# Kernel tuning notes

Hardware: AMD Instinct MI355X
Metric: run time of the kernel (lower is better)

Reference implementation:

```python
import jax, jax.numpy as jnp
import numpy as np
import math

B, S, D = 4, 1024, 1024
E, DE = 8, 128            # n_experts, expert_dim (D == E*DE)
TOPK = 2
SCALE = 1.0 / math.sqrt(D)  # source divides by sqrt(self.dim) = sqrt(transformer_dim)


def setup_inputs() -> dict:
    key = jax.random.key(0)
    k1, k2, k3, k4, k5 = jax.random.split(key, 5)
    Q = jax.random.normal(k1, (B, S, D), dtype=jnp.float32)
    K = jax.random.normal(k2, (B, S, D), dtype=jnp.float32)
    V = jax.random.normal(k3, (B, S, D), dtype=jnp.float32)
    route_prob = jax.random.uniform(k4, (B, E), dtype=jnp.float32)
    # first-stage MoE dispatch (idx_list): expert_mask[e, b] == 1 iff batch b routed to expert e
    expert_mask = jax.random.randint(k5, (E, B), 0, 2).astype(jnp.int32)
    mask = jnp.ones((B, S), dtype=jnp.float32)  # accepted but unused by the source forward
    return {"Q": Q, "K": K, "V": V, "route_prob": route_prob,
            "expert_mask": expert_mask, "mask": mask}


def reference(Q, K, V, route_prob, expert_mask, mask):
    # RowParallelMatmulWithMoE: each expert e attends using its 128-wide feature slice
    Qe = Q.reshape(B, S, E, DE)
    Ke = K.reshape(B, S, E, DE)
    scores = jnp.einsum('bsed,bted->ebst', Qe, Ke) * SCALE   # [E, B, S, S]
    probs = jax.nn.softmax(scores, axis=-1)                   # per-expert softmax (dropout p=0)
    # index_add_ scatter: sum routed experts' attention maps per batch element
    m1 = expert_mask.astype(Q.dtype)                          # [E, B]
    attn = jnp.einsum('eb,ebst->bst', m1, probs)              # [B, S, S]
    # preprocess: top-k expert re-selection from route_prob -> new idx_list
    _, top_idx = jax.lax.top_k(route_prob, TOPK)              # [B, TOPK]
    m2 = jnp.zeros((B, E), dtype=Q.dtype).at[jnp.arange(B)[:, None], top_idx].set(1.0)
    # ColumnParallelMatmulWithMoE: attn @ V restricted to each selected expert's V slice
    Ve = V.reshape(B, S, E, DE)
    out = jnp.einsum('bst,bted->bsed', attn, Ve) * m2[:, None, :, None]  # [B, S, E, DE]
    return out.reshape(B, S, D)
```

## Files before the change

kernel.cpp:

```cpp
#include <hip/hip_runtime.h>
#include <hip/hip_bf16.h>
#include <stdint.h>

#define B_ 4
#define S_ 1024
#define E_ 8
#define DE_ 128
#define SCALE_ 0.03125f

typedef __attribute__((ext_vector_type(8))) short short8;
typedef __attribute__((ext_vector_type(4))) float f32x4;
typedef unsigned short ushort_t;
typedef unsigned int uint32;
typedef unsigned long long u64;
typedef unsigned char uchar;

__device__ __forceinline__ ushort_t f2bf(float f) {
    uint32 u = __float_as_uint(f);
    uint32 r = u + 0x7fffu + ((u >> 16) & 1u);
    return (ushort_t)(r >> 16);
}

__device__ __forceinline__ uchar f2fp8(float f) {
    float a = fminf(fmaxf(f, -448.f), 448.f);
    uint32 u = __float_as_uint(a);
    uint32 s = (u >> 31) << 7;
    int ex = (int)((u >> 23) & 0xff);
    uint32 man = u & 0x7fffff;
    int e8 = ex - 127 + 7;
    if (e8 >= 1) {
        uint32 m = man >> 20;
        uint32 rem = man & 0xfffff;
        if (rem > 0x80000u || (rem == 0x80000u && (m & 1))) ++m;
        if (m == 8) { m = 0; ++e8; }
        if (e8 > 15) { e8 = 15; m = 6; }
        return (uchar)(s | ((uint32)e8 << 3) | m);
    } else {
        int m = (int)rintf(fabsf(a) * 512.f);
        if (m > 7) m = 7;
        return (uchar)(s | (uint32)m);
    }
}

#define GLOAD_LDS16(g, l) __builtin_amdgcn_global_load_lds( \
    (const __attribute__((address_space(1))) unsigned int*)(g), \
    (__attribute__((address_space(3))) unsigned int*)(l), 16, 0, 0)

__device__ __forceinline__ void stageK32(const uchar* g, uchar* lds, int tid) {
    #pragma unroll
    for (int k2 = 0; k2 < 4; ++k2) {
        int u = tid + k2 * 512;
        int r = u >> 3, c = u & 7;
        int cc = c ^ (r & 7);
        GLOAD_LDS16(g + r * 128 + (cc << 4), lds + (u << 4));
    }
}
__device__ __forceinline__ void stageV32(const uchar* g, uchar* lds, int tid) {
    #pragma unroll
    for (int k2 = 0; k2 < 4; ++k2) {
        int u = tid + k2 * 512;
        int r = u >> 4, c = u & 15;
        int cc = (c & 8) | ((c & 7) ^ (r & 7));
        GLOAD_LDS16(g + (size_t)r * 2048 + (cc << 4), lds + (u << 4));
    }
}
__device__ __forceinline__ void stageQ(const uchar* g, uchar* lds, int tid) {
    if (tid < 128) {
        int r = tid >> 3, c = tid & 7;
        int cc = c ^ (r & 7);
        GLOAD_LDS16(g + r * 128 + (cc << 4), lds + (tid << 4));
    }
}
__device__ __forceinline__ u64 fld8(const uchar* lds, int row, int kk, int quad) {
    int c = kk * 2 + (quad >> 1);
    int phys = c ^ (row & 7);
    return *(const u64*)(lds + row * 128 + (phys << 4) + ((quad & 1) << 3));
}
__device__ __forceinline__ short8 fldv(const uchar* lds, int row, int kk, int quad) {
    int c = kk * 4 + quad;
    int phys = (c & 8) | ((c & 7) ^ (row & 7));
    return *(const short8*)(lds + (size_t)row * 256 + (phys << 4));
}

__device__ __forceinline__ void top2(const float* rp, int& i1, int& i2) {
    float v1 = rp[0]; i1 = 0;
    #pragma unroll
    for (int i = 1; i < 8; ++i) { float v = rp[i]; if (v > v1) { v1 = v; i1 = i; } }
    float v2 = -1e30f; i2 = 0;
    #pragma unroll
    for (int i = 0; i < 8; ++i) {
        if (i == i1) continue;
        float v = rp[i]; if (v > v2) { v2 = v; i2 = i; }
    }
}

__global__ __launch_bounds__(256) void prep_kernel(
        const float* __restrict__ Q, const float* __restrict__ K,
        const float* __restrict__ V, const float* __restrict__ route,
        const int* __restrict__ em,
        uchar* __restrict__ Qb, uchar* __restrict__ Kb,
        ushort_t* __restrict__ Vt, float* __restrict__ out) {
    __shared__ ushort_t tile[64][130];
    const int tid = threadIdx.x;
    const int sc = blockIdx.x, e = blockIdx.y, b = blockIdx.z;
    const int s0 = sc * 64;
    const size_t plane8 = ((size_t)(b * 8 + e)) << 17;

    const bool ak = em[e * B_ + b] != 0;
    int i1, i2; top2(route + b * 8, i1, i2);
    const bool av = (e == i1) || (e == i2);

    if (!av) {
        #pragma unroll
        for (int i = 0; i < 8; ++i) {
            int idx = tid + i * 256, r = idx >> 5, c4 = idx & 31;
            *(float4*)(out + (((size_t)(b * 1024 + s0 + r)) << 10) + (e << 7) + (c4 << 2))
                = make_float4(0.f, 0.f, 0.f, 0.f);
        }
    }
    if (ak) {
        #pragma unroll
        for (int i = 0; i < 2; ++i) {
            int u = tid + i * 256;
            int r = u >> 3, dg = u & 7;
            const float* qs = Q + ((size_t)(b * 1024 + s0 + r) << 10) + (e << 7) + (dg << 4);
            const float* ks = K + ((size_t)(b * 1024 + s0 + r) << 10) + (e << 7) + (dg << 4);
            union { uint4 w; uchar c[16]; } oq, ok;
            #pragma unroll
            for (int j = 0; j < 4; ++j) {
                float4 qv = ((const float4*)qs)[j];
                float4 kv = ((const float4*)ks)[j];
                oq.c[j*4+0] = f2fp8(qv.x); oq.c[j*4+1] = f2fp8(qv.y);
                oq.c[j*4+2] = f2fp8(qv.z); oq.c[j*4+3] = f2fp8(qv.w);
                ok.c[j*4+0] = f2fp8(kv.x); ok.c[j*4+1] = f2fp8(kv.y);
                ok.c[j*4+2] = f2fp8(kv.z); ok.c[j*4+3] = f2fp8(kv.w);
            }
            size_t oo = plane8 + ((size_t)(s0 + r) << 7) + (dg << 4);
            *(uint4*)(Qb + oo) = oq.w;
            *(uint4*)(Kb + oo) = ok.w;
        }
    }
    if (av) {
        #pragma unroll
        for (int i = 0; i < 8; ++i) {
            int idx = tid + i * 256, r = idx >> 5, c4 = idx & 31;
            size_t in_off = ((size_t)(b * 1024 + s0 + r) << 10) + (e << 7) + (c4 << 2);
            float4 v = *(const float4*)(V + in_off);
            ushort_t* p = &tile[r][c4 << 2];
            p[0] = f2bf(v.x); p[1] = f2bf(v.y); p[2] = f2bf(v.z); p[3] = f2bf(v.w);
        }
        __syncthreads();
        #pragma unroll
        for (int i = 0; i < 4; ++i) {
            int item = tid + i * 256, d = item & 127, sg = item >> 7;
            union { uint4 q; ushort_t u[8]; } tmp;
            #pragma unroll
            for (int j = 0; j < 8; ++j) tmp.u[j] = tile[sg * 8 + j][d];
            *(uint4*)(Vt + (((size_t)(b * 8 + e)) << 17) + (((size_t)d) << 10)
                      + s0 + (sg << 3)) = tmp.q;
        }
    }
}

__global__ __launch_bounds__(512, 1) void attn_mega(
        const uchar* __restrict__ Qb, const uchar* __restrict__ Kb,
        const ushort_t* __restrict__ Vt, const float* __restrict__ route,
        const int* __restrict__ em, float* __restrict__ out) {

    __shared__ __align__(16) uchar kt[2][32768];
    __shared__ __align__(16) uchar qt[2][2048];
    __shared__ __align__(16) uchar attnL[32768];
    __shared__ float red[8][16];

    const int stile = blockIdx.x, b = blockIdx.y;
    const int s0 = stile * 16;
    const int tid = threadIdx.x;
    const int w = tid >> 6, lane = tid & 63;
    const int quad = lane >> 4, l16 = lane & 15;

    uint32 epack = 0; int ne = 0;
    #pragma unroll
    for (int e = 0; e < 8; ++e)
        if (em[e * B_ + b] != 0) { epack |= (uint32)e << (3 * ne); ++ne; }
    int i1, i2; top2(route + b * 8, i1, i2);

    f32x4 aacc[4][2];
    #pragma unroll
    for (int c = 0; c < 4; ++c)
        #pragma unroll
        for (int n = 0; n < 2; ++n) aacc[c][n] = (f32x4){0.f, 0.f, 0.f, 0.f};

    if (ne > 0) {
        int e0 = epack & 7;
        stageQ(Qb + (((size_t)(b * 8 + e0)) << 17) + ((size_t)s0 << 7), qt[0], tid);
        stageK32(Kb + (((size_t)(b * 8 + e0)) << 17), kt[0], tid);
        __syncthreads();

        for (int i = 0; i < ne; ++i) {
            int e = (epack >> (3 * i)) & 7;
            const uchar* kp = Kb + (((size_t)(b * 8 + e)) << 17);

            u64 af[4];
            #pragma unroll
            for (int kk = 0; kk < 4; ++kk) af[kk] = fld8(qt[i & 1], l16, kk, quad);

            float rsum[4] = {0.f, 0.f, 0.f, 0.f};
            f32x4 ps[4][2];

            #pragma unroll
            for (int c = 0; c < 4; ++c) {
                int g = i * 4 + c;
                if (c < 3) {
                    stageK32(kp + (size_t)(c + 1) * 32768, kt[(g + 1) & 1], tid);
                } else if (i + 1 < ne) {
                    int en = (epack >> (3 * (i + 1))) & 7;
                    stageQ(Qb + (((size_t)(b * 8 + en)) << 17) + ((size_t)s0 << 7),
                           qt[(i + 1) & 1], tid);
                    stageK32(Kb + (((size_t)(b * 8 + en)) << 17), kt[(g + 1) & 1], tid);
                } else {
                    stageV32((const uchar*)(Vt + (((size_t)(b * 8 + i1)) << 17)),
                             kt[(g + 1) & 1], tid);
                }
                const uchar* kb = kt[g & 1];
                #pragma unroll
                for (int n = 0; n < 2; ++n) {
                    f32x4 s = {0.f, 0.f, 0.f, 0.f};
                    int trow = w * 32 + n * 16 + l16;
                    #pragma unroll
                    for (int kk = 0; kk < 4; ++kk) {
                        u64 bf = fld8(kb, trow, kk, quad);
                        s = __builtin_amdgcn_mfma_f32_16x16x32_fp8_fp8(
                            (long)af[kk], (long)bf, s, 0, 0, 0);
                    }
                    #pragma unroll
                    for (int r = 0; r < 4; ++r) {
                        float p = __expf(s[r] * SCALE_);
                        ps[c][n][r] = p;
                        rsum[r] += p;
                    }
                }
                __syncthreads();
            }

            #pragma unroll
            for (int off = 1; off < 16; off <<= 1)
                #pragma unroll
                for (int r = 0; r < 4; ++r) rsum[r] += __shfl_xor(rsum[r], off, 64);
            if (l16 == 0) {
                #pragma unroll
                for (int r = 0; r < 4; ++r) red[w][quad * 4 + r] = rsum[r];
            }
            __syncthreads();
            float rinv[4];
            #pragma unroll
            for (int r = 0; r < 4; ++r) {
                float l = 0.f;
                #pragma unroll
                for (int ww = 0; ww < 8; ++ww) l += red[ww][quad * 4 + r];
                rinv[r] = 1.0f / l;
            }
            #pragma unroll
            for (int c = 0; c < 4; ++c)
                #pragma unroll
                for (int n = 0; n < 2; ++n)
                    #pragma unroll
                    for (int r = 0; r < 4; ++r)
                        aacc[c][n][r] += ps[c][n][r] * rinv[r];
        }
    } else {
        stageV32((const uchar*)(Vt + (((size_t)(b * 8 + i1)) << 17)), kt[0], tid);
    }

    #pragma unroll
    for (int c = 0; c < 4; ++c)
        #pragma unroll
        for (int n = 0; n < 2; ++n)
            #pragma unroll
            for (int r = 0; r < 4; ++r) {
                int row = quad * 4 + r;
                int t = c * 256 + w * 32 + n * 16 + l16;
                int ct = t >> 3;
                int phys = (ct & ~7) | ((ct & 7) ^ (row & 7));
                *(ushort_t*)(attnL + row * 2048 + (phys << 4) + ((t & 7) << 1)) =
                    f2bf(aacc[c][n][r]);
            }
    __syncthreads();

    int selE[2] = {i1, i2};
    #pragma unroll
    for (int sel = 0; sel < 2; ++sel) {
        const uchar* vp = (const uchar*)(Vt + (((size_t)(b * 8 + selE[sel])) << 17));
        f32x4 oacc = {0.f, 0.f, 0.f, 0.f};
        #pragma unroll
        for (int c = 0; c < 8; ++c) {
            int g = ne * 4 + sel * 8 + c;
            if (c < 7)
                stageV32(vp + (size_t)(c + 1) * 256, kt[(g + 1) & 1], tid);
            else if (sel == 0)
                stageV32((const uchar*)(Vt + (((size_t)(b * 8 + selE[1])) << 17)),
                         kt[(g + 1) & 1], tid);
            const uchar* vb = kt[g & 1];
            #pragma unroll
            for (int kk = 0; kk < 4; ++kk) {
                int ct = c * 16 + kk * 4 + quad;
                int phys = (ct & ~7) | ((ct & 7) ^ (l16 & 7));
                short8 afr = *(const short8*)(attnL + l16 * 2048 + (phys << 4));
                short8 bfr = fldv(vb, w * 16 + l16, kk, quad);
                oacc = __builtin_amdgcn_mfma_f32_16x16x32_bf16(afr, bfr, oacc, 0, 0, 0);
            }
            __syncthreads();
        }
        #pragma unroll
        for (int r = 0; r < 4; ++r)
            out[(((size_t)(b * 1024 + s0 + quad * 4 + r)) << 10)
                + selE[sel] * 128 + w * 16 + l16] = oacc[r];
    }
}

extern "C" void kernel_launch(void* const* d_in, const int* in_sizes, int n_in,
                              void* d_out, int out_size, void* d_ws, size_t ws_size,
                              hipStream_t stream) {
    const float* Q     = (const float*)d_in[0];
    const float* K     = (const float*)d_in[1];
    const float* V     = (const float*)d_in[2];
    const float* route = (const float*)d_in[3];
    const int*   em    = (const int*)d_in[4];
    float* out = (float*)d_out;

    const size_t NB = (size_t)B_ * E_ * S_ * DE_;
    uchar* Qb = (uchar*)d_ws;
    uchar* Kb = Qb + NB;
    ushort_t* Vt = (ushort_t*)(Kb + NB);

    dim3 gp(16, 8, 4);
    prep_kernel<<<gp, 256, 0, stream>>>(Q, K, V, route, em, Qb, Kb, Vt, out);
    dim3 gm(64, 4);
    attn_mega<<<gm, 512, 0, stream>>>(Qb, Kb, Vt, route, em, out);
}
```

Measured before the change: 135.8 us.

## Triple-buffer K/V staging with vmcnt-based waits and preload all Q tiles

Moves from a double-buffered LDS ring to a triple-buffered one that keeps two stages in flight. Each stage waits with s_waitcnt vmcnt(4) plus a raw s_barrier instead of a full __syncthreads, so the next global-to-LDS load no longer waits for all loads to drain. All routed experts' Q tiles are loaded up front with 4-byte LDS-direct loads spread over all threads, and output stores are deferred to the end. This uses more LDS (96KB ring plus 16KB Q), and correctness depends on the hand-counted vmcnt matching the per-thread load count.

```diff
diff --git a/kernel.cpp b/kernel.cpp
--- a/kernel.cpp
+++ b/kernel.cpp
@@ -45,6 +45,9 @@
 #define GLOAD_LDS16(g, l) __builtin_amdgcn_global_load_lds( \
     (const __attribute__((address_space(1))) unsigned int*)(g), \
     (__attribute__((address_space(3))) unsigned int*)(l), 16, 0, 0)
+#define GLOAD_LDS4(g, l) __builtin_amdgcn_global_load_lds( \
+    (const __attribute__((address_space(1))) unsigned int*)(g), \
+    (__attribute__((address_space(3))) unsigned int*)(l), 4, 0, 0)
 
 __device__ __forceinline__ void stageK32(const uchar* g, uchar* lds, int tid) {
     #pragma unroll
@@ -64,12 +67,12 @@
         GLOAD_LDS16(g + (size_t)r * 2048 + (cc << 4), lds + (u << 4));
     }
 }
-__device__ __forceinline__ void stageQ(const uchar* g, uchar* lds, int tid) {
-    if (tid < 128) {
-        int r = tid >> 3, c = tid & 7;
-        int cc = c ^ (r & 7);
-        GLOAD_LDS16(g + r * 128 + (cc << 4), lds + (tid << 4));
-    }
+__device__ __forceinline__ void stageQ4(const uchar* g, uchar* lds, int tid) {
+    int r = tid >> 5;
+    int ct = (tid >> 2) & 7;
+    int bo = (tid & 3) << 2;
+    int cc = ct ^ (r & 7);
+    GLOAD_LDS4(g + r * 128 + (cc << 4) + bo, lds + (tid << 2));
 }
 __device__ __forceinline__ u64 fld8(const uchar* lds, int row, int kk, int quad) {
     int c = kk * 2 + (quad >> 1);
@@ -167,8 +170,8 @@
         const ushort_t* __restrict__ Vt, const float* __restrict__ route,
         const int* __restrict__ em, float* __restrict__ out) {
 
-    __shared__ __align__(16) uchar kt[2][32768];
-    __shared__ __align__(16) uchar qt[2][2048];
+    __shared__ __align__(16) uchar kt3[3 * 32768];
+    __shared__ __align__(16) uchar qAll[16384];
     __shared__ __align__(16) uchar attnL[32768];
     __shared__ float red[8][16];
 
@@ -184,91 +187,109 @@
         if (em[e * B_ + b] != 0) { epack |= (uint32)e << (3 * ne); ++ne; }
     int i1, i2; top2(route + b * 8, i1, i2);
 
+    const int tk = ne * 4;
+    const int G = tk + 16;
+
     f32x4 aacc[4][2];
     #pragma unroll
     for (int c = 0; c < 4; ++c)
         #pragma unroll
         for (int n = 0; n < 2; ++n) aacc[c][n] = (f32x4){0.f, 0.f, 0.f, 0.f};
 
-    if (ne > 0) {
-        int e0 = epack & 7;
-        stageQ(Qb + (((size_t)(b * 8 + e0)) << 17) + ((size_t)s0 << 7), qt[0], tid);
-        stageK32(Kb + (((size_t)(b * 8 + e0)) << 17), kt[0], tid);
-        __syncthreads();
-
-        for (int i = 0; i < ne; ++i) {
-            int e = (epack >> (3 * i)) & 7;
-            const uchar* kp = Kb + (((size_t)(b * 8 + e)) << 17);
-
-            u64 af[4];
-            #pragma unroll
-            for (int kk = 0; kk < 4; ++kk) af[kk] = fld8(qt[i & 1], l16, kk, quad);
-
-            float rsum[4] = {0.f, 0.f, 0.f, 0.f};
-            f32x4 ps[4][2];
-
-            #pragma unroll
-            for (int c = 0; c < 4; ++c) {
-                int g = i * 4 + c;
-                if (c < 3) {
-                    stageK32(kp + (size_t)(c + 1) * 32768, kt[(g + 1) & 1], tid);
-                } else if (i + 1 < ne) {
-                    int en = (epack >> (3 * (i + 1))) & 7;
-                    stageQ(Qb + (((size_t)(b * 8 + en)) << 17) + ((size_t)s0 << 7),
-                           qt[(i + 1) & 1], tid);
-                    stageK32(Kb + (((size_t)(b * 8 + en)) << 17), kt[(g + 1) & 1], tid);
-                } else {
-                    stageV32((const uchar*)(Vt + (((size_t)(b * 8 + i1)) << 17)),
-                             kt[(g + 1) & 1], tid);
+    int ib = 0;
+    int cb = 0;
+
+    auto issue = [&](int g) {
+        uchar* buf = kt3 + (size_t)ib * 32768u;
+        if (g < tk) {
+            int e = (epack >> (3 * (g >> 2))) & 7;
+            stageK32(Kb + (((size_t)(b * 8 + e)) << 17) + (size_t)(g & 3) * 32768,
+                     buf, tid);
+        } else {
+            int v = g - tk;
+            int e = (v >> 3) ? i2 : i1;
+            stageV32((const uchar*)(Vt + (((size_t)(b * 8 + e)) << 17))
+                         + (size_t)(v & 7) * 256,
+                     buf, tid);
+        }
+        ib = (ib == 2) ? 0 : ib + 1;
+    };
+    auto pipe = [&](int g) {
+        if (g + 1 < G) asm volatile("s_waitcnt vmcnt(4)" ::: "memory");
+        else           asm volatile("s_waitcnt vmcnt(0)" ::: "memory");
+        __builtin_amdgcn_s_barrier();
+        __builtin_amdgcn_sched_barrier(0);
+        if (g + 2 < G) issue(g + 2);
+    };
+
+    for (int i = 0; i < ne; ++i) {
+        int e = (epack >> (3 * i)) & 7;
+        stageQ4(Qb + (((size_t)(b * 8 + e)) << 17) + ((size_t)s0 << 7),
+                qAll + i * 2048, tid);
+    }
+    issue(0); issue(1);
+
+    for (int i = 0; i < ne; ++i) {
+        const uchar* qp = qAll + i * 2048;
+        u64 af[4];
+        float rsum[4] = {0.f, 0.f, 0.f, 0.f};
+        f32x4 ps[4][2];
+
+        #pragma unroll
+        for (int c = 0; c < 4; ++c) {
+            int g = i * 4 + c;
+            pipe(g);
+            if (c == 0) {
+                #pragma unroll
+                for (int kk = 0; kk < 4; ++kk) af[kk] = fld8(qp, l16, kk, quad);
+            }
+            const uchar* kb = kt3 + (size_t)cb * 32768u;
+            cb = (cb == 2) ? 0 : cb + 1;
+            #pragma unroll
+            for (int n = 0; n < 2; ++n) {
+                f32x4 s = {0.f, 0.f, 0.f, 0.f};
+                int trow = w * 32 + n * 16 + l16;
+                #pragma unroll
+                for (int kk = 0; kk < 4; ++kk) {
+                    u64 bf = fld8(kb, trow, kk, quad);
+                    s = __builtin_amdgcn_mfma_f32_16x16x32_fp8_fp8(
+                        (long)af[kk], (long)bf, s, 0, 0, 0);
                 }
-                const uchar* kb = kt[g & 1];
                 #pragma unroll
-                for (int n = 0; n < 2; ++n) {
-                    f32x4 s = {0.f, 0.f, 0.f, 0.f};
-                    int trow = w * 32 + n * 16 + l16;
-                    #pragma unroll
-                    for (int kk = 0; kk < 4; ++kk) {
-                        u64 bf = fld8(kb, trow, kk, quad);
-                        s = __builtin_amdgcn_mfma_f32_16x16x32_fp8_fp8(
-                            (long)af[kk], (long)bf, s, 0, 0, 0);
-                    }
-                    #pragma unroll
-                    for (int r = 0; r < 4; ++r) {
-                        float p = __expf(s[r] * SCALE_);
-                        ps[c][n][r] = p;
-                        rsum[r] += p;
-                    }
+                for (int r = 0; r < 4; ++r) {
+                    float p = __expf(s[r] * SCALE_);
+                    ps[c][n][r] = p;
+                    rsum[r] += p;
                 }
-                __syncthreads();
-            }
-
-            #pragma unroll
-            for (int off = 1; off < 16; off <<= 1)
+            }
+        }
+
+        #pragma unroll
+        for (int off = 1; off < 16; off <<= 1)
+            #pragma unroll
+            for (int r = 0; r < 4; ++r) rsum[r] += __shfl_xor(rsum[r], off, 64);
+        if (l16 == 0) {
+            #pragma unroll
+            for (int r = 0; r < 4; ++r) red[w][quad * 4 + r] = rsum[r];
+        }
+        asm volatile("s_waitcnt lgkmcnt(0)" ::: "memory");
+        __builtin_amdgcn_s_barrier();
+        __builtin_amdgcn_sched_barrier(0);
+        float rinv[4];
+        #pragma unroll
+        for (int r = 0; r < 4; ++r) {
+            float l = 0.f;
+            #pragma unroll
+            for (int ww = 0; ww < 8; ++ww) l += red[ww][quad * 4 + r];
+            rinv[r] = 1.0f / l;
+        }
+        #pragma unroll
+        for (int c = 0; c < 4; ++c)
+            #pragma unroll
+            for (int n = 0; n < 2; ++n)
                 #pragma unroll
-                for (int r = 0; r < 4; ++r) rsum[r] += __shfl_xor(rsum[r], off, 64);
-            if (l16 == 0) {
-                #pragma unroll
-                for (int r = 0; r < 4; ++r) red[w][quad * 4 + r] = rsum[r];
-            }
-            __syncthreads();
-            float rinv[4];
-            #pragma unroll
-            for (int r = 0; r < 4; ++r) {
-                float l = 0.f;
-                #pragma unroll
-                for (int ww = 0; ww < 8; ++ww) l += red[ww][quad * 4 + r];
-                rinv[r] = 1.0f / l;
-            }
-            #pragma unroll
-            for (int c = 0; c < 4; ++c)
-                #pragma unroll
-                for (int n = 0; n < 2; ++n)
-                    #pragma unroll
-                    for (int r = 0; r < 4; ++r)
-                        aacc[c][n][r] += ps[c][n][r] * rinv[r];
-        }
-    } else {
-        stageV32((const uchar*)(Vt + (((size_t)(b * 8 + i1)) << 17)), kt[0], tid);
+                for (int r = 0; r < 4; ++r)
+                    aacc[c][n][r] += ps[c][n][r] * rinv[r];
     }
 
     #pragma unroll
@@ -284,37 +305,40 @@
                 *(ushort_t*)(attnL + row * 2048 + (phys << 4) + ((t & 7) << 1)) =
                     f2bf(aacc[c][n][r]);
             }
-    __syncthreads();
+    asm volatile("s_waitcnt lgkmcnt(0)" ::: "memory");
+    __builtin_amdgcn_s_barrier();
+    __builtin_amdgcn_sched_barrier(0);
 
     int selE[2] = {i1, i2};
+    f32x4 oacc[2];
+    #pragma unroll
+    for (int sel = 0; sel < 2; ++sel) oacc[sel] = (f32x4){0.f, 0.f, 0.f, 0.f};
+
     #pragma unroll
     for (int sel = 0; sel < 2; ++sel) {
-        const uchar* vp = (const uchar*)(Vt + (((size_t)(b * 8 + selE[sel])) << 17));
-        f32x4 oacc = {0.f, 0.f, 0.f, 0.f};
         #pragma unroll
         for (int c = 0; c < 8; ++c) {
-            int g = ne * 4 + sel * 8 + c;
-            if (c < 7)
-                stageV32(vp + (size_t)(c + 1) * 256, kt[(g + 1) & 1], tid);
-            else if (sel == 0)
-                stageV32((const uchar*)(Vt + (((size_t)(b * 8 + selE[1])) << 17)),
-                         kt[(g + 1) & 1], tid);
-            const uchar* vb = kt[g & 1];
+            int g = tk + sel * 8 + c;
+            pipe(g);
+            const uchar* vb = kt3 + (size_t)cb * 32768u;
+            cb = (cb == 2) ? 0 : cb + 1;
             #pragma unroll
             for (int kk = 0; kk < 4; ++kk) {
                 int ct = c * 16 + kk * 4 + quad;
                 int phys = (ct & ~7) | ((ct & 7) ^ (l16 & 7));
                 short8 afr = *(const short8*)(attnL + l16 * 2048 + (phys << 4));
                 short8 bfr = fldv(vb, w * 16 + l16, kk, quad);
-                oacc = __builtin_amdgcn_mfma_f32_16x16x32_bf16(afr, bfr, oacc, 0, 0, 0);
-            }
-            __syncthreads();
-        }
+                oacc[sel] = __builtin_amdgcn_mfma_f32_16x16x32_bf16(
+                    afr, bfr, oacc[sel], 0, 0, 0);
+            }
+        }
+    }
+    #pragma unroll
+    for (int sel = 0; sel < 2; ++sel)
         #pragma unroll
         for (int r = 0; r < 4; ++r)
             out[(((size_t)(b * 1024 + s0 + quad * 4 + r)) << 10)
-                + selE[sel] * 128 + w * 16 + l16] = oacc[r];
-    }
+                + selE[sel] * 128 + w * 16 + l16] = oacc[sel][r];
 }
 
 extern "C" void kernel_launch(void* const* d_in, const int* in_sizes, int n_in,
```

Result: no change. 135.3 us (-0.3%).

## Load K, Q and V MFMA fragments directly from global memory, dropping LDS staging

Applied to the files above, without the earlier changes.

Removes the double-buffered LDS staging of K, Q and V tiles (global_load_lds plus swizzled LDS reads and per-chunk barriers) and has each lane load its MFMA fragments straight from global memory. This cuts LDS usage from about 100KB to about 33KB and removes most __syncthreads. The softmax reduction buffer is double-buffered so no trailing barrier is needed. The cost is that global loads are now 8 or 16 bytes per lane with strided rows, they are no longer prefetched ahead of compute, and any reuse across waves has to come from the L1/L2 caches.

```diff
diff --git a/kernel.cpp b/kernel.cpp
--- a/kernel.cpp
+++ b/kernel.cpp
@@ -42,46 +42,6 @@
     }
 }
 
-#define GLOAD_LDS16(g, l) __builtin_amdgcn_global_load_lds( \
-    (const __attribute__((address_space(1))) unsigned int*)(g), \
-    (__attribute__((address_space(3))) unsigned int*)(l), 16, 0, 0)
-
-__device__ __forceinline__ void stageK32(const uchar* g, uchar* lds, int tid) {
-    #pragma unroll
-    for (int k2 = 0; k2 < 4; ++k2) {
-        int u = tid + k2 * 512;
-        int r = u >> 3, c = u & 7;
-        int cc = c ^ (r & 7);
-        GLOAD_LDS16(g + r * 128 + (cc << 4), lds + (u << 4));
-    }
-}
-__device__ __forceinline__ void stageV32(const uchar* g, uchar* lds, int tid) {
-    #pragma unroll
-    for (int k2 = 0; k2 < 4; ++k2) {
-        int u = tid + k2 * 512;
-        int r = u >> 4, c = u & 15;
-        int cc = (c & 8) | ((c & 7) ^ (r & 7));
-        GLOAD_LDS16(g + (size_t)r * 2048 + (cc << 4), lds + (u << 4));
-    }
-}
-__device__ __forceinline__ void stageQ(const uchar* g, uchar* lds, int tid) {
-    if (tid < 128) {
-        int r = tid >> 3, c = tid & 7;
-        int cc = c ^ (r & 7);
-        GLOAD_LDS16(g + r * 128 + (cc << 4), lds + (tid << 4));
-    }
-}
-__device__ __forceinline__ u64 fld8(const uchar* lds, int row, int kk, int quad) {
-    int c = kk * 2 + (quad >> 1);
-    int phys = c ^ (row & 7);
-    return *(const u64*)(lds + row * 128 + (phys << 4) + ((quad & 1) << 3));
-}
-__device__ __forceinline__ short8 fldv(const uchar* lds, int row, int kk, int quad) {
-    int c = kk * 4 + quad;
-    int phys = (c & 8) | ((c & 7) ^ (row & 7));
-    return *(const short8*)(lds + (size_t)row * 256 + (phys << 4));
-}
-
 __device__ __forceinline__ void top2(const float* rp, int& i1, int& i2) {
     float v1 = rp[0]; i1 = 0;
     #pragma unroll
@@ -167,10 +127,8 @@
         const ushort_t* __restrict__ Vt, const float* __restrict__ route,
         const int* __restrict__ em, float* __restrict__ out) {
 
-    __shared__ __align__(16) uchar kt[2][32768];
-    __shared__ __align__(16) uchar qt[2][2048];
     __shared__ __align__(16) uchar attnL[32768];
-    __shared__ float red[8][16];
+    __shared__ float red[2][8][16];
 
     const int stile = blockIdx.x, b = blockIdx.y;
     const int s0 = stile * 16;
@@ -190,85 +148,67 @@
         #pragma unroll
         for (int n = 0; n < 2; ++n) aacc[c][n] = (f32x4){0.f, 0.f, 0.f, 0.f};
 
-    if (ne > 0) {
-        int e0 = epack & 7;
-        stageQ(Qb + (((size_t)(b * 8 + e0)) << 17) + ((size_t)s0 << 7), qt[0], tid);
-        stageK32(Kb + (((size_t)(b * 8 + e0)) << 17), kt[0], tid);
+    for (int i = 0; i < ne; ++i) {
+        int e = (epack >> (3 * i)) & 7;
+        const uchar* kp = Kb + (((size_t)(b * 8 + e)) << 17);
+        const uchar* qp = Qb + (((size_t)(b * 8 + e)) << 17) + ((size_t)s0 << 7)
+                          + l16 * 128 + quad * 8;
+
+        u64 af[4];
+        #pragma unroll
+        for (int kk = 0; kk < 4; ++kk) af[kk] = *(const u64*)(qp + kk * 32);
+
+        float rsum[4] = {0.f, 0.f, 0.f, 0.f};
+        f32x4 ps[4][2];
+
+        #pragma unroll
+        for (int c = 0; c < 4; ++c) {
+            #pragma unroll
+            for (int n = 0; n < 2; ++n) {
+                int trow = c * 256 + w * 32 + n * 16 + l16;
+                const uchar* krow = kp + (size_t)trow * 128 + quad * 8;
+                u64 b0 = *(const u64*)(krow);
+                u64 b1 = *(const u64*)(krow + 32);
+                u64 b2 = *(const u64*)(krow + 64);
+                u64 b3 = *(const u64*)(krow + 96);
+                f32x4 s = {0.f, 0.f, 0.f, 0.f};
+                s = __builtin_amdgcn_mfma_f32_16x16x32_fp8_fp8((long)af[0], (long)b0, s, 0, 0, 0);
+                s = __builtin_amdgcn_mfma_f32_16x16x32_fp8_fp8((long)af[1], (long)b1, s, 0, 0, 0);
+                s = __builtin_amdgcn_mfma_f32_16x16x32_fp8_fp8((long)af[2], (long)b2, s, 0, 0, 0);
+                s = __builtin_amdgcn_mfma_f32_16x16x32_fp8_fp8((long)af[3], (long)b3, s, 0, 0, 0);
+                #pragma unroll
+                for (int r = 0; r < 4; ++r) {
+                    float p = __expf(s[r] * SCALE_);
+                    ps[c][n][r] = p;
+                    rsum[r] += p;
+                }
+            }
+        }
+
+        #pragma unroll
+        for (int off = 1; off < 16; off <<= 1)
+            #pragma unroll
+            for (int r = 0; r < 4; ++r) rsum[r] += __shfl_xor(rsum[r], off, 64);
+        if (l16 == 0) {
+            #pragma unroll
+            for (int r = 0; r < 4; ++r) red[i & 1][w][quad * 4 + r] = rsum[r];
+        }
         __syncthreads();
-
-        for (int i = 0; i < ne; ++i) {
-            int e = (epack >> (3 * i)) & 7;
-            const uchar* kp = Kb + (((size_t)(b * 8 + e)) << 17);
-
-            u64 af[4];
-            #pragma unroll
-            for (int kk = 0; kk < 4; ++kk) af[kk] = fld8(qt[i & 1], l16, kk, quad);
-
-            float rsum[4] = {0.f, 0.f, 0.f, 0.f};
-            f32x4 ps[4][2];
-
-            #pragma unroll
-            for (int c = 0; c < 4; ++c) {
-                int g = i * 4 + c;
-                if (c < 3) {
-                    stageK32(kp + (size_t)(c + 1) * 32768, kt[(g + 1) & 1], tid);
-                } else if (i + 1 < ne) {
-                    int en = (epack >> (3 * (i + 1))) & 7;
-                    stageQ(Qb + (((size_t)(b * 8 + en)) << 17) + ((size_t)s0 << 7),
-                           qt[(i + 1) & 1], tid);
-                    stageK32(Kb + (((size_t)(b * 8 + en)) << 17), kt[(g + 1) & 1], tid);
-                } else {
-                    stageV32((const uchar*)(Vt + (((size_t)(b * 8 + i1)) << 17)),
-                             kt[(g + 1) & 1], tid);
-                }
-                const uchar* kb = kt[g & 1];
+        float rinv[4];
+        #pragma unroll
+        for (int r = 0; r < 4; ++r) {
+            float l = 0.f;
+            #pragma unroll
+            for (int ww = 0; ww < 8; ++ww) l += red[i & 1][ww][quad * 4 + r];
+            rinv[r] = 1.0f / l;
+        }
+        #pragma unroll
+        for (int c = 0; c < 4; ++c)
+            #pragma unroll
+            for (int n = 0; n < 2; ++n)
                 #pragma unroll
-                for (int n = 0; n < 2; ++n) {
-                    f32x4 s = {0.f, 0.f, 0.f, 0.f};
-                    int trow = w * 32 + n * 16 + l16;
-                    #pragma unroll
-                    for (int kk = 0; kk < 4; ++kk) {
-                        u64 bf = fld8(kb, trow, kk, quad);
-                        s = __builtin_amdgcn_mfma_f32_16x16x32_fp8_fp8(
-                            (long)af[kk], (long)bf, s, 0, 0, 0);
-                    }
-                    #pragma unroll
-                    for (int r = 0; r < 4; ++r) {
-                        float p = __expf(s[r] * SCALE_);
-                        ps[c][n][r] = p;
-                        rsum[r] += p;
-                    }
-                }
-                __syncthreads();
-            }
-
-            #pragma unroll
-            for (int off = 1; off < 16; off <<= 1)
-                #pragma unroll
-                for (int r = 0; r < 4; ++r) rsum[r] += __shfl_xor(rsum[r], off, 64);
-            if (l16 == 0) {
-                #pragma unroll
-                for (int r = 0; r < 4; ++r) red[w][quad * 4 + r] = rsum[r];
-            }
-            __syncthreads();
-            float rinv[4];
-            #pragma unroll
-            for (int r = 0; r < 4; ++r) {
-                float l = 0.f;
-                #pragma unroll
-                for (int ww = 0; ww < 8; ++ww) l += red[ww][quad * 4 + r];
-                rinv[r] = 1.0f / l;
-            }
-            #pragma unroll
-            for (int c = 0; c < 4; ++c)
-                #pragma unroll
-                for (int n = 0; n < 2; ++n)
-                    #pragma unroll
-                    for (int r = 0; r < 4; ++r)
-                        aacc[c][n][r] += ps[c][n][r] * rinv[r];
-        }
-    } else {
-        stageV32((const uchar*)(Vt + (((size_t)(b * 8 + i1)) << 17)), kt[0], tid);
+                for (int r = 0; r < 4; ++r)
+                    aacc[c][n][r] += ps[c][n][r] * rinv[r];
     }
 
     #pragma unroll
@@ -289,26 +229,19 @@
     int selE[2] = {i1, i2};
     #pragma unroll
     for (int sel = 0; sel < 2; ++sel) {
-        const uchar* vp = (const uchar*)(Vt + (((size_t)(b * 8 + selE[sel])) << 17));
+        const uchar* vrow = (const uchar*)(Vt + (((size_t)(b * 8 + selE[sel])) << 17))
+                            + (size_t)(w * 16 + l16) * 2048 + quad * 16;
         f32x4 oacc = {0.f, 0.f, 0.f, 0.f};
         #pragma unroll
         for (int c = 0; c < 8; ++c) {
-            int g = ne * 4 + sel * 8 + c;
-            if (c < 7)
-                stageV32(vp + (size_t)(c + 1) * 256, kt[(g + 1) & 1], tid);
-            else if (sel == 0)
-                stageV32((const uchar*)(Vt + (((size_t)(b * 8 + selE[1])) << 17)),
-                         kt[(g + 1) & 1], tid);
-            const uchar* vb = kt[g & 1];
             #pragma unroll
             for (int kk = 0; kk < 4; ++kk) {
                 int ct = c * 16 + kk * 4 + quad;
                 int phys = (ct & ~7) | ((ct & 7) ^ (l16 & 7));
                 short8 afr = *(const short8*)(attnL + l16 * 2048 + (phys << 4));
-                short8 bfr = fldv(vb, w * 16 + l16, kk, quad);
+                short8 bfr = *(const short8*)(vrow + c * 256 + kk * 64);
                 oacc = __builtin_amdgcn_mfma_f32_16x16x32_bf16(afr, bfr, oacc, 0, 0, 0);
             }
-            __syncthreads();
         }
         #pragma unroll
         for (int r = 0; r < 4; ++r)
```

Result: slower. 165.4 us (+21.8%).
